# Performance work log

Hardware: AMD Instinct MI355X
Metric: run time of the kernel (lower is better)

The kernel has to match this reference:

```python
import jax, jax.numpy as jnp
import numpy as np

S = 14          # grid size
L_COORD = 5.0
L_NOOBJ = 0.5
BATCH = 4096


def setup_inputs() -> dict:
    key = jax.random.key(0)
    k1, k2, k3 = jax.random.split(key, 3)
    shape = (BATCH, S, S, 30)
    # strictly positive values so sqrt(w), sqrt(h) are well defined (as assumed by the torch code)
    pred = jax.random.uniform(k1, shape, dtype=jnp.float32, minval=0.01, maxval=1.0)
    target = jax.random.uniform(k2, shape, dtype=jnp.float32, minval=0.01, maxval=1.0)
    has_obj = (jax.random.uniform(k3, (BATCH, S, S)) < 0.3).astype(jnp.float32)
    target = target.at[..., 4].set(has_obj)
    return {"pred_tensor": pred, "target_tensor": target}


def _yolo_loss(pred_tensor, target_tensor):
    N = pred_tensor.shape[0]
    dt = pred_tensor.dtype

    obj = (target_tensor[..., 4] > 0).astype(dt)      # [N,S,S]
    noobj = (target_tensor[..., 4] == 0).astype(dt)   # [N,S,S]

    # ---- no-object confidence loss (channels 4 and 9 in cells without objects) ----
    d4 = pred_tensor[..., 4] - target_tensor[..., 4]
    d9 = pred_tensor[..., 9] - target_tensor[..., 9]
    no_object_loss = jnp.sum(noobj * (d4 * d4 + d9 * d9))

    # ---- class prediction loss (channels 10:30 in object cells) ----
    dcls = pred_tensor[..., 10:] - target_tensor[..., 10:]
    class_loss = jnp.sum(obj[..., None] * dcls * dcls)

    # ---- per-cell best-IoU box selection (vectorized over all cells) ----
    pboxes = pred_tensor[..., :10].reshape(N, S, S, 2, 5)    # [N,S,S,2,5]
    tboxes = target_tensor[..., :10].reshape(N, S, S, 2, 5)
    p = pboxes[..., :4]                                      # [N,S,S,2,4]
    t = tboxes[..., 0, :4]                                   # target box of the cell [N,S,S,4]

    # [x,y,w,h] (center+size, xy in grid units) -> corner coords
    p1 = p[..., :2] / S - p[..., 2:] / 2                     # [N,S,S,2,2]
    p2 = p[..., :2] / S + p[..., 2:] / 2
    t1 = t[..., :2] / S - t[..., 2:] / 2                     # [N,S,S,2]
    t2 = t[..., :2] / S + t[..., 2:] / 2

    lt = jnp.maximum(p1, t1[..., None, :])
    rb = jnp.minimum(p2, t2[..., None, :])
    wh = jnp.maximum(rb - lt, 0.0)
    inter = wh[..., 0] * wh[..., 1]                          # [N,S,S,2]
    area_p = (p2[..., 0] - p1[..., 0]) * (p2[..., 1] - p1[..., 1])
    area_t = ((t2[..., 0] - t1[..., 0]) * (t2[..., 1] - t1[..., 1]))[..., None]
    iou = inter / (area_p + area_t - inter)                  # [N,S,S,2]

    # torch code: if IoU[0] > IoU[1] pick box 0 else box 1 (ties -> box 1)
    pick1 = iou[..., 0] <= iou[..., 1]                       # [N,S,S] bool
    p_sel = jnp.where(pick1[..., None], pboxes[..., 1, :], pboxes[..., 0, :])  # [N,S,S,5]
    t_sel = jnp.where(pick1[..., None], tboxes[..., 1, :], tboxes[..., 0, :])
    iou_best = jnp.where(pick1, iou[..., 1], iou[..., 0])    # [N,S,S]

    dxy = p_sel[..., :2] - t_sel[..., :2]
    dwh = jnp.sqrt(p_sel[..., 2:4]) - jnp.sqrt(t_sel[..., 2:4])
    reg_loss = jnp.sum(obj[..., None] * dxy * dxy) + jnp.sum(obj[..., None] * dwh * dwh)

    # ---- containing-object confidence loss: pred conf vs best IoU ----
    dconf = p_sel[..., 4] - iou_best
    contain_loss = jnp.sum(obj * dconf * dconf)

    total = L_NOOBJ * no_object_loss + class_loss + L_COORD * reg_loss + contain_loss
    return total / N


def reference(pred_tensor, target_tensor):
    return _yolo_loss(pred_tensor, target_tensor)
```

## Files before the change

### kernel.cpp

```cpp
#include <hip/hip_runtime.h>

#define SDIM 14
#define L_COORD 5.0f
#define L_NOOBJ 0.5f
#define BATCH 4096
#define CELLS (BATCH * SDIM * SDIM)
#define BLOCK 256
#define CPB 256
#define NBLOCKS (CELLS / CPB)
#define BSTR 11

__global__ __launch_bounds__(BLOCK) void yolo_loss(
    const float* __restrict__ pred, const float* __restrict__ targ,
    float* __restrict__ out) {
    __shared__ float bP[CPB * BSTR];
    __shared__ float bT[CPB * BSTR];
    __shared__ float cls[CPB];
    __shared__ float wsum[BLOCK / 64];

    const int tid = threadIdx.x;
    cls[tid] = 0.0f;
    __syncthreads();

    const size_t base2 = (size_t)blockIdx.x * (CPB * 30 / 2);
    const float2* p2 = reinterpret_cast<const float2*>(pred) + base2;
    const float2* t2 = reinterpret_cast<const float2*>(targ) + base2;

#pragma unroll
    for (int j = 0; j < 15; ++j) {
        const int idx = tid + j * BLOCK;
        const float2 pv = p2[idx];
        const float2 tv = t2[idx];
        const int e0 = idx * 2;
        const int cell = e0 / 30;
        const int ch = e0 - cell * 30;
        if (ch < 10) {
            const int o = cell * BSTR + ch;
            bP[o] = pv.x; bP[o + 1] = pv.y;
            bT[o] = tv.x; bT[o + 1] = tv.y;
        } else {
            const float d0 = pv.x - tv.x;
            const float d1 = pv.y - tv.y;
            atomicAdd(&cls[cell], d0 * d0 + d1 * d1);
        }
    }
    __syncthreads();

    const float* P = bP + tid * BSTR;
    const float* T = bT + tid * BSTR;
    const float obj = T[4];
    const float noobj = 1.0f - obj;

    const float invS = 1.0f / (float)SDIM;
    const float t1x = T[0] * invS - T[2] * 0.5f;
    const float t1y = T[1] * invS - T[3] * 0.5f;
    const float t2x = T[0] * invS + T[2] * 0.5f;
    const float t2y = T[1] * invS + T[3] * 0.5f;
    const float area_t = (t2x - t1x) * (t2y - t1y);

    float iou0 = 0.0f, iou1 = 0.0f;
#pragma unroll
    for (int k = 0; k < 2; ++k) {
        const float bx = P[5 * k + 0], by = P[5 * k + 1];
        const float bw = P[5 * k + 2], bh = P[5 * k + 3];
        const float p1x = bx * invS - bw * 0.5f;
        const float p1y = by * invS - bh * 0.5f;
        const float p2x = bx * invS + bw * 0.5f;
        const float p2y = by * invS + bh * 0.5f;
        const float ltx = fmaxf(p1x, t1x), lty = fmaxf(p1y, t1y);
        const float rbx = fminf(p2x, t2x), rby = fminf(p2y, t2y);
        const float wx = fmaxf(rbx - ltx, 0.0f);
        const float wy = fmaxf(rby - lty, 0.0f);
        const float inter = wx * wy;
        const float area_p = (p2x - p1x) * (p2y - p1y);
        const float v = inter / (area_p + area_t - inter);
        if (k == 0) iou0 = v; else iou1 = v;
    }
    const bool pick1 = (iou0 <= iou1);
    const float iou_best = pick1 ? iou1 : iou0;
    const float psx = pick1 ? P[5] : P[0];
    const float psy = pick1 ? P[6] : P[1];
    const float psw = pick1 ? P[7] : P[2];
    const float psh = pick1 ? P[8] : P[3];
    const float psc = pick1 ? P[9] : P[4];
    const float tsx = pick1 ? T[5] : T[0];
    const float tsy = pick1 ? T[6] : T[1];
    const float tsw = pick1 ? T[7] : T[2];
    const float tsh = pick1 ? T[8] : T[3];

    const float dx = psx - tsx, dy = psy - tsy;
    const float dw = sqrtf(psw) - sqrtf(tsw);
    const float dh = sqrtf(psh) - sqrtf(tsh);
    const float reg = dx * dx + dy * dy + dw * dw + dh * dh;
    const float dconf = psc - iou_best;
    const float d4 = P[4] - T[4];
    const float d9 = P[9] - T[9];

    float loss = obj * (cls[tid] + L_COORD * reg + dconf * dconf)
               + L_NOOBJ * noobj * (d4 * d4 + d9 * d9);

#pragma unroll
    for (int off = 32; off > 0; off >>= 1)
        loss += __shfl_down(loss, off, 64);
    const int lane = tid & 63;
    const int wave = tid >> 6;
    if (lane == 0) wsum[wave] = loss;
    __syncthreads();
    if (tid == 0) {
        const float bsum = wsum[0] + wsum[1] + wsum[2] + wsum[3];
        atomicAdd(out, bsum * (1.0f / (float)BATCH));
    }
}

extern "C" void kernel_launch(void* const* d_in, const int* in_sizes, int n_in,
                              void* d_out, int out_size, void* d_ws, size_t ws_size,
                              hipStream_t stream) {
    const float* pred = (const float*)d_in[0];
    const float* targ = (const float*)d_in[1];
    float* out = (float*)d_out;

    hipMemsetAsync(out, 0, sizeof(float), stream);
    yolo_loss<<<NBLOCKS, BLOCK, 0, stream>>>(pred, targ, out);
}
```

Baseline: 231.2 us.

## Stage full cell data into LDS via direct global-to-LDS loads

Replaces the per-thread float2 loads, which scattered box channels into padded shared arrays and sent class-channel partial sums through shared-memory atomics, with 16-byte global_load_lds transfers that copy the block's full pred and target tiles straight into LDS. Each thread then reads its own 30-channel cell from LDS and computes the class loss itself, so the integer div/mod and the LDS atomics are gone. The cost is twice the LDS footprint (about 60KB per block), which limits occupancy, and a stride-30 per-thread LDS read pattern that can cause bank conflicts.

New measurement: 206.1 us. -10.8%, faster.

```diff
diff --git a/kernel.cpp b/kernel.cpp
--- a/kernel.cpp
+++ b/kernel.cpp
@@ -8,48 +8,41 @@
 #define BLOCK 256
 #define CPB 256
 #define NBLOCKS (CELLS / CPB)
-#define BSTR 11
+#define BLK_F 7680
 
 __global__ __launch_bounds__(BLOCK) void yolo_loss(
     const float* __restrict__ pred, const float* __restrict__ targ,
     float* __restrict__ out) {
-    __shared__ float bP[CPB * BSTR];
-    __shared__ float bT[CPB * BSTR];
-    __shared__ float cls[CPB];
+    __shared__ float s[2 * BLK_F];
     __shared__ float wsum[BLOCK / 64];
 
     const int tid = threadIdx.x;
-    cls[tid] = 0.0f;
-    __syncthreads();
-
-    const size_t base2 = (size_t)blockIdx.x * (CPB * 30 / 2);
-    const float2* p2 = reinterpret_cast<const float2*>(pred) + base2;
-    const float2* t2 = reinterpret_cast<const float2*>(targ) + base2;
+    const int wave = tid >> 6;
+    const int lane = tid & 63;
+    const size_t blockbase = (size_t)blockIdx.x * BLK_F;
 
 #pragma unroll
-    for (int j = 0; j < 15; ++j) {
-        const int idx = tid + j * BLOCK;
-        const float2 pv = p2[idx];
-        const float2 tv = t2[idx];
-        const int e0 = idx * 2;
-        const int cell = e0 / 30;
-        const int ch = e0 - cell * 30;
-        if (ch < 10) {
-            const int o = cell * BSTR + ch;
-            bP[o] = pv.x; bP[o + 1] = pv.y;
-            bT[o] = tv.x; bT[o + 1] = tv.y;
-        } else {
-            const float d0 = pv.x - tv.x;
-            const float d1 = pv.y - tv.y;
-            atomicAdd(&cls[cell], d0 * d0 + d1 * d1);
-        }
+    for (int i = 0; i < 15; ++i) {
+        const int c = wave + i * 4;
+        const float* gsrc = (c < 30)
+            ? (pred + blockbase + (size_t)c * 256)
+            : (targ + blockbase + (size_t)(c - 30) * 256);
+        __builtin_amdgcn_global_load_lds(
+            (const __attribute__((address_space(1))) void*)(gsrc + lane * 4),
+            (__attribute__((address_space(3))) void*)(s + c * 256),
+            16, 0, 0);
     }
     __syncthreads();
 
-    const float* P = bP + tid * BSTR;
-    const float* T = bT + tid * BSTR;
+    const float* P = s + tid * 30;
+    const float* T = s + BLK_F + tid * 30;
+
     const float obj = T[4];
     const float noobj = 1.0f - obj;
+
+    float cls = 0.0f;
+#pragma unroll
+    for (int c = 10; c < 30; ++c) { const float d = P[c] - T[c]; cls += d * d; }
 
     const float invS = 1.0f / (float)SDIM;
     const float t1x = T[0] * invS - T[2] * 0.5f;
@@ -96,14 +89,12 @@
     const float d4 = P[4] - T[4];
     const float d9 = P[9] - T[9];
 
-    float loss = obj * (cls[tid] + L_COORD * reg + dconf * dconf)
+    float loss = obj * (cls + L_COORD * reg + dconf * dconf)
                + L_NOOBJ * noobj * (d4 * d4 + d9 * d9);
 
 #pragma unroll
     for (int off = 32; off > 0; off >>= 1)
         loss += __shfl_down(loss, off, 64);
-    const int lane = tid & 63;
-    const int wave = tid >> 6;
     if (lane == 0) wsum[wave] = loss;
     __syncthreads();
     if (tid == 0) {
```
